# Optimization experiments

Measured on AMD Instinct MI355X. Metric: run time of the kernel, lower is better.

Reference implementation:

```python
import jax, jax.numpy as jnp
import numpy as np

NUM_EMBEDDINGS = 1024
EMBEDDING_DIM = 64
COMMITMENT_COST = 0.25

def setup_inputs() -> dict:
    key = jax.random.key(0)
    k1, k2 = jax.random.split(key)
    z = jax.random.normal(k1, (64, EMBEDDING_DIM, 32, 32), dtype=jnp.float32)
    # nn.Embedding initialized uniform(-1/K, 1/K)
    lim = 1.0 / NUM_EMBEDDINGS
    embeddings = jax.random.uniform(k2, (NUM_EMBEDDINGS, EMBEDDING_DIM), dtype=jnp.float32, minval=-lim, maxval=lim)
    return {"z": z, "embeddings": embeddings}

def reference(z, embeddings):
    # z: [B, C, H, W] with C == embedding_dim
    z_perm = jnp.transpose(z, (0, 2, 3, 1))            # [B, H, W, D]
    flat_z = z_perm.reshape(-1, EMBEDDING_DIM)          # [N, D]
    # squared L2 distances: ||z||^2 - 2 z.e + ||e||^2  -> [N, K]
    distances = (jnp.sum(flat_z ** 2, axis=1, keepdims=True)
                 - 2.0 * flat_z @ embeddings.T
                 + jnp.sum(embeddings ** 2, axis=1))
    encoding_indices = jnp.argmin(distances, axis=1)    # [N]
    # direct gather == one-hot @ embeddings (same math, no [N,K] one-hot)
    quantized = embeddings[encoding_indices].reshape(z_perm.shape)
    commitment_loss = COMMITMENT_COST * jnp.mean((jax.lax.stop_gradient(quantized) - z_perm) ** 2)
    codebook_loss = jnp.mean((quantized - jax.lax.stop_gradient(z_perm)) ** 2)
    loss = commitment_loss + codebook_loss
    # straight-through estimator
    quantized_st = z_perm + jax.lax.stop_gradient(quantized - z_perm)
    return jnp.transpose(quantized_st, (0, 3, 1, 2)), loss
```

## Files before the change

kernel.cpp:

```cpp
#include <hip/hip_runtime.h>

#define D 64
#define K 1024
#define NVEC 65536
#define MB 128
#define NBLK (NVEC / MB)
#define WAVES 4
#define KPW (K / WAVES)
#define TILES (KPW / 16)
#define NG (MB / 16)
#define RING 4

typedef __attribute__((ext_vector_type(8))) short bf16x8;
typedef __attribute__((ext_vector_type(4))) float f32x4;

__device__ inline unsigned pk2t(float a, float b) {
    return __builtin_amdgcn_perm(__builtin_bit_cast(unsigned, b),
                                 __builtin_bit_cast(unsigned, a), 0x07060302u);
}
__device__ inline int max3i(int a, int b, int c) {
    const int m = a > b ? a : b;
    return m > c ? m : c;
}

__global__ __launch_bounds__(256) void vq_prep(const float* __restrict__ emb,
                                               unsigned* __restrict__ ebf_u,
                                               float* __restrict__ hb) {
    const int r = blockIdx.x * 8 + (threadIdx.x >> 5);
    const int j = threadIdx.x & 31;
    const float2 v = *reinterpret_cast<const float2*>(emb + (size_t)r * D + j * 2);
    ebf_u[(size_t)r * 32 + j] = pk2t(v.x, v.y);
    float s = fmaf(v.x, v.x, v.y * v.y);
#pragma unroll
    for (int off = 1; off < 32; off <<= 1) s += __shfl_xor(s, off, 64);
    if (j == 0) hb[r] = 1.0f - 0.5f * s;
}

__global__ __launch_bounds__(256, 2) void vq_main(const float* __restrict__ z,
                                                  const float* __restrict__ emb,
                                                  const unsigned short* __restrict__ ebf,
                                                  const float* __restrict__ hb,
                                                  float* __restrict__ out,
                                                  float* __restrict__ pP) {
    __shared__ __align__(16) char zl[MB * 128];
    __shared__ int   wv[WAVES * MB];
    __shared__ int   fin[MB];
    __shared__ float redw[WAVES];

    const int tid = threadIdx.x;
    const int blk = blockIdx.x;
    const int b   = blk >> 3;
    const int hw0 = (blk & 7) * MB;
    const float* zb = z + (size_t)b * (D * 1024) + hw0;

    const int wave = tid >> 6;
    const int lane = tid & 63;
    const int cw   = wave * KPW;
    const int l16  = lane & 15;
    const int lg   = lane >> 4;

    float zacc = 0.f;
#pragma unroll
    for (int it = 0; it < 2; ++it) {
        const int item = it * 256 + tid;
        const int v4 = item & 31;
        const int d4 = item >> 5;
        float4 r[4];
#pragma unroll
        for (int i = 0; i < 4; ++i)
            r[i] = *reinterpret_cast<const float4*>(zb + (size_t)(d4 * 4 + i) * 1024 + v4 * 4);
        const float* rf = reinterpret_cast<const float*>(r);
#pragma unroll
        for (int n = 0; n < 16; ++n) zacc = fmaf(rf[n], rf[n], zacc);
#pragma unroll
        for (int j = 0; j < 4; ++j) {
            const int v = v4 * 4 + j;
            uint2 pk;
            pk.x = pk2t(rf[0 * 4 + j], rf[1 * 4 + j]);
            pk.y = pk2t(rf[2 * 4 + j], rf[3 * 4 + j]);
            const int byte = v * 128 + ((d4 * 8) ^ ((v & 7) << 4));
            *reinterpret_cast<uint2*>(zl + byte) = pk;
        }
    }

    bf16x8 A0[RING], A1[RING];
    f32x4  CI[RING];
#pragma unroll
    for (int p = 0; p < RING; ++p) {
        const unsigned short* row = ebf + (size_t)(cw + p * 16 + l16) * 64;
        A0[p] = *reinterpret_cast<const bf16x8*>(row + lg * 8);
        A1[p] = *reinterpret_cast<const bf16x8*>(row + 32 + lg * 8);
        CI[p] = *reinterpret_cast<const f32x4*>(hb + cw + p * 16 + lg * 4);
    }
    __syncthreads();

    bf16x8 bfr[NG][2];
#pragma unroll
    for (int g = 0; g < NG; ++g)
#pragma unroll
        for (int h = 0; h < 2; ++h) {
            const int v = g * 16 + l16;
            const int byte = v * 128 + (((h * 64) + lg * 16) ^ ((v & 7) << 4));
            bfr[g][h] = *reinterpret_cast<const bf16x8*>(zl + byte);
        }

    int best[NG];
#pragma unroll
    for (int g = 0; g < NG; ++g) best[g] = 0;

#pragma unroll 4
    for (int kt = 0; kt < TILES; ++kt) {
        const int cur = kt & (RING - 1);
        const bf16x8 b0 = A0[cur], b1 = A1[cur];
        const f32x4  cc = CI[cur];
        const int nk = (kt + RING < TILES) ? kt + RING : kt;
        const unsigned short* nrow = ebf + (size_t)(cw + nk * 16 + l16) * 64;
        A0[cur] = *reinterpret_cast<const bf16x8*>(nrow + lg * 8);
        A1[cur] = *reinterpret_cast<const bf16x8*>(nrow + 32 + lg * 8);
        CI[cur] = *reinterpret_cast<const f32x4*>(hb + cw + nk * 16 + lg * 4);

        const int idx0 = cw + kt * 16 + lg * 4;
#pragma unroll
        for (int g = 0; g < NG; ++g) {
            f32x4 c = cc;
            c = __builtin_amdgcn_mfma_f32_16x16x32_bf16(b0, bfr[g][0], c, 0, 0, 0);
            c = __builtin_amdgcn_mfma_f32_16x16x32_bf16(b1, bfr[g][1], c, 0, 0, 0);
            const int p0 = (int)((__builtin_bit_cast(unsigned, c[0]) & 0xFFFFFC00u) | (unsigned)(idx0 + 0));
            const int p1 = (int)((__builtin_bit_cast(unsigned, c[1]) & 0xFFFFFC00u) | (unsigned)(idx0 + 1));
            const int p2 = (int)((__builtin_bit_cast(unsigned, c[2]) & 0xFFFFFC00u) | (unsigned)(idx0 + 2));
            const int p3 = (int)((__builtin_bit_cast(unsigned, c[3]) & 0xFFFFFC00u) | (unsigned)(idx0 + 3));
            best[g] = max3i(max3i(p0, p1, p2), p3, best[g]);
        }
    }

#pragma unroll
    for (int g = 0; g < NG; ++g) {
        int tv = best[g];
        int o = __shfl_xor(tv, 16, 64); tv = tv > o ? tv : o;
        o = __shfl_xor(tv, 32, 64);     tv = tv > o ? tv : o;
        if (lane < 16) wv[wave * MB + g * 16 + l16] = tv;
    }
    __syncthreads();

    float tcon = 0.f;
    if (tid < MB) {
        int tv = wv[tid];
#pragma unroll
        for (int w = 1; w < WAVES; ++w) {
            const int o = wv[w * MB + tid];
            tv = tv > o ? tv : o;
        }
        fin[tid] = tv & (K - 1);
        tcon = __builtin_bit_cast(float, (unsigned)tv & 0xFFFFFC00u) - 1.0f;
    }
    __syncthreads();

    {
        const int v  = tid & 127;
        const int dh = tid >> 7;
        const int idx = fin[v];
        const float4* eq4 = reinterpret_cast<const float4*>(emb + (size_t)idx * D + dh * 32);
        float* ob = out + (size_t)b * (D * 1024) + hw0 + v;
#pragma unroll
        for (int i = 0; i < 8; ++i) {
            const float4 q = eq4[i];
            const int d = dh * 32 + i * 4;
            ob[(size_t)(d + 0) * 1024] = q.x;
            ob[(size_t)(d + 1) * 1024] = q.y;
            ob[(size_t)(d + 2) * 1024] = q.z;
            ob[(size_t)(d + 3) * 1024] = q.w;
        }
    }

    float s = zacc - 2.f * tcon;
#pragma unroll
    for (int off = 1; off < 64; off <<= 1) s += __shfl_xor(s, off, 64);
    if (lane == 0) redw[wave] = s;
    __syncthreads();
    if (tid == 0) pP[blk] = (redw[0] + redw[1]) + (redw[2] + redw[3]);
}

__global__ __launch_bounds__(256) void vq_loss(const float* __restrict__ pP,
                                               float* __restrict__ loss_out) {
    __shared__ float red[256];
    float s = 0.f;
    for (int i = threadIdx.x; i < NBLK; i += 256) s += pP[i];
    red[threadIdx.x] = s;
    __syncthreads();
#pragma unroll
    for (int st = 128; st > 0; st >>= 1) {
        if (threadIdx.x < st) red[threadIdx.x] += red[threadIdx.x + st];
        __syncthreads();
    }
    if (threadIdx.x == 0)
        loss_out[0] = 1.25f * red[0] * (1.0f / (float)((size_t)NVEC * D));
}

extern "C" void kernel_launch(void* const* d_in, const int* in_sizes, int n_in,
                              void* d_out, int out_size, void* d_ws, size_t ws_size,
                              hipStream_t stream) {
    const float* z   = (const float*)d_in[0];
    const float* emb = (const float*)d_in[1];
    float* out = (float*)d_out;

    char* ws = (char*)d_ws;
    unsigned* ebf_u = (unsigned*)ws;
    float* hb = (float*)(ws + 131072);
    float* pP = (float*)(ws + 135168);

    vq_prep<<<128, 256, 0, stream>>>(emb, ebf_u, hb);
    vq_main<<<NBLK, 256, 0, stream>>>(z, emb, (const unsigned short*)ebf_u, hb, out, pP);
    vq_loss<<<1, 256, 0, stream>>>(pP, out + (size_t)NVEC * D);
}
```

Baseline: 29.05 us.

## Fuse codebook bf16 conversion and norm computation into main kernel, drop prep launch

Removes the separate prep kernel that converted the codebook to bf16 and computed per-code half-norms. The main kernel now loads fp32 codebook rows directly, packs them to bf16 in registers and computes the norms with shuffles inside the k-tile loop. This saves one kernel launch and its workspace round trip, but every one of the 512 blocks now redoes the conversion and norm work and reads twice as many codebook bytes. The prefetch ring is reduced from 4 to 2 to offset the larger fp32 register footprint.

```diff
diff --git a/kernel.cpp b/kernel.cpp
--- a/kernel.cpp
+++ b/kernel.cpp
@@ -9,10 +9,11 @@
 #define KPW (K / WAVES)
 #define TILES (KPW / 16)
 #define NG (MB / 16)
-#define RING 4
+#define RING 2
 
 typedef __attribute__((ext_vector_type(8))) short bf16x8;
 typedef __attribute__((ext_vector_type(4))) float f32x4;
+typedef __attribute__((ext_vector_type(4))) int i32x4;
 
 __device__ inline unsigned pk2t(float a, float b) {
     return __builtin_amdgcn_perm(__builtin_bit_cast(unsigned, b),
@@ -22,24 +23,14 @@
     const int m = a > b ? a : b;
     return m > c ? m : c;
 }
-
-__global__ __launch_bounds__(256) void vq_prep(const float* __restrict__ emb,
-                                               unsigned* __restrict__ ebf_u,
-                                               float* __restrict__ hb) {
-    const int r = blockIdx.x * 8 + (threadIdx.x >> 5);
-    const int j = threadIdx.x & 31;
-    const float2 v = *reinterpret_cast<const float2*>(emb + (size_t)r * D + j * 2);
-    ebf_u[(size_t)r * 32 + j] = pk2t(v.x, v.y);
-    float s = fmaf(v.x, v.x, v.y * v.y);
-#pragma unroll
-    for (int off = 1; off < 32; off <<= 1) s += __shfl_xor(s, off, 64);
-    if (j == 0) hb[r] = 1.0f - 0.5f * s;
+__device__ inline float dot4(float4 v, float acc) {
+    acc = fmaf(v.x, v.x, acc); acc = fmaf(v.y, v.y, acc);
+    acc = fmaf(v.z, v.z, acc); acc = fmaf(v.w, v.w, acc);
+    return acc;
 }
 
 __global__ __launch_bounds__(256, 2) void vq_main(const float* __restrict__ z,
                                                   const float* __restrict__ emb,
-                                                  const unsigned short* __restrict__ ebf,
-                                                  const float* __restrict__ hb,
                                                   float* __restrict__ out,
                                                   float* __restrict__ pP) {
     __shared__ __align__(16) char zl[MB * 128];
@@ -83,14 +74,12 @@
         }
     }
 
-    bf16x8 A0[RING], A1[RING];
-    f32x4  CI[RING];
+    float4 F0[RING], F1[RING], F2[RING], F3[RING];
 #pragma unroll
     for (int p = 0; p < RING; ++p) {
-        const unsigned short* row = ebf + (size_t)(cw + p * 16 + l16) * 64;
-        A0[p] = *reinterpret_cast<const bf16x8*>(row + lg * 8);
-        A1[p] = *reinterpret_cast<const bf16x8*>(row + 32 + lg * 8);
-        CI[p] = *reinterpret_cast<const f32x4*>(hb + cw + p * 16 + lg * 4);
+        const float4* rp = reinterpret_cast<const float4*>(emb + (size_t)(cw + p * 16 + l16) * D);
+        F0[p] = rp[lg * 2];     F1[p] = rp[lg * 2 + 1];
+        F2[p] = rp[8 + lg * 2]; F3[p] = rp[8 + lg * 2 + 1];
     }
     __syncthreads();
 
@@ -108,23 +97,36 @@
 #pragma unroll
     for (int g = 0; g < NG; ++g) best[g] = 0;
 
-#pragma unroll 4
+#pragma unroll 2
     for (int kt = 0; kt < TILES; ++kt) {
         const int cur = kt & (RING - 1);
-        const bf16x8 b0 = A0[cur], b1 = A1[cur];
-        const f32x4  cc = CI[cur];
+        const float4 f0 = F0[cur], f1 = F1[cur], f2 = F2[cur], f3 = F3[cur];
         const int nk = (kt + RING < TILES) ? kt + RING : kt;
-        const unsigned short* nrow = ebf + (size_t)(cw + nk * 16 + l16) * 64;
-        A0[cur] = *reinterpret_cast<const bf16x8*>(nrow + lg * 8);
-        A1[cur] = *reinterpret_cast<const bf16x8*>(nrow + 32 + lg * 8);
-        CI[cur] = *reinterpret_cast<const f32x4*>(hb + cw + nk * 16 + lg * 4);
+        const float4* np = reinterpret_cast<const float4*>(emb + (size_t)(cw + nk * 16 + l16) * D);
+        F0[cur] = np[lg * 2];     F1[cur] = np[lg * 2 + 1];
+        F2[cur] = np[8 + lg * 2]; F3[cur] = np[8 + lg * 2 + 1];
+
+        i32x4 ai0 = { (int)pk2t(f0.x, f0.y), (int)pk2t(f0.z, f0.w),
+                      (int)pk2t(f1.x, f1.y), (int)pk2t(f1.z, f1.w) };
+        i32x4 ai1 = { (int)pk2t(f2.x, f2.y), (int)pk2t(f2.z, f2.w),
+                      (int)pk2t(f3.x, f3.y), (int)pk2t(f3.z, f3.w) };
+        const bf16x8 a0 = __builtin_bit_cast(bf16x8, ai0);
+        const bf16x8 a1 = __builtin_bit_cast(bf16x8, ai1);
+
+        float nrm = dot4(f3, dot4(f2, dot4(f1, dot4(f0, 0.f))));
+        nrm += __shfl_xor(nrm, 16, 64);
+        nrm += __shfl_xor(nrm, 32, 64);
+        f32x4 cc;
+#pragma unroll
+        for (int r = 0; r < 4; ++r)
+            cc[r] = fmaf(-0.5f, __shfl(nrm, lg * 4 + r, 16), 1.0f);
 
         const int idx0 = cw + kt * 16 + lg * 4;
 #pragma unroll
         for (int g = 0; g < NG; ++g) {
             f32x4 c = cc;
-            c = __builtin_amdgcn_mfma_f32_16x16x32_bf16(b0, bfr[g][0], c, 0, 0, 0);
-            c = __builtin_amdgcn_mfma_f32_16x16x32_bf16(b1, bfr[g][1], c, 0, 0, 0);
+            c = __builtin_amdgcn_mfma_f32_16x16x32_bf16(a0, bfr[g][0], c, 0, 0, 0);
+            c = __builtin_amdgcn_mfma_f32_16x16x32_bf16(a1, bfr[g][1], c, 0, 0, 0);
             const int p0 = (int)((__builtin_bit_cast(unsigned, c[0]) & 0xFFFFFC00u) | (unsigned)(idx0 + 0));
             const int p1 = (int)((__builtin_bit_cast(unsigned, c[1]) & 0xFFFFFC00u) | (unsigned)(idx0 + 1));
             const int p2 = (int)((__builtin_bit_cast(unsigned, c[2]) & 0xFFFFFC00u) | (unsigned)(idx0 + 2));
@@ -203,12 +205,8 @@
     const float* emb = (const float*)d_in[1];
     float* out = (float*)d_out;
 
-    char* ws = (char*)d_ws;
-    unsigned* ebf_u = (unsigned*)ws;
-    float* hb = (float*)(ws + 131072);
-    float* pP = (float*)(ws + 135168);
-
-    vq_prep<<<128, 256, 0, stream>>>(emb, ebf_u, hb);
-    vq_main<<<NBLK, 256, 0, stream>>>(z, emb, (const unsigned short*)ebf_u, hb, out, pP);
+    float* pP = (float*)d_ws;
+
+    vq_main<<<NBLK, 256, 0, stream>>>(z, emb, out, pP);
     vq_loss<<<1, 256, 0, stream>>>(pP, out + (size_t)NVEC * D);
 }
```

After: 29.63 us. About the same (+2.0%).

## Fuse loss reduction into main kernel via last-block atomic counter

Applied to the files above, without the earlier changes.

Drops the separate single-block loss kernel. Each block now publishes its partial sum atomically and bumps a global counter, and the last block to arrive does the final reduction. This removes one kernel launch and its serialization gap. The register prefetch ring is also cut from 4 to 2 with a smaller unroll, which lowers register pressure but shortens latency hiding for codebook loads. The counter is never reset and relies on a modulo of the block count, so it assumes the workspace starts at zero and NBLK is a power of two.

```diff
diff --git a/kernel.cpp b/kernel.cpp
--- a/kernel.cpp
+++ b/kernel.cpp
@@ -9,7 +9,7 @@
 #define KPW (K / WAVES)
 #define TILES (KPW / 16)
 #define NG (MB / 16)
-#define RING 4
+#define RING 2
 
 typedef __attribute__((ext_vector_type(8))) short bf16x8;
 typedef __attribute__((ext_vector_type(4))) float f32x4;
@@ -41,11 +41,14 @@
                                                   const unsigned short* __restrict__ ebf,
                                                   const float* __restrict__ hb,
                                                   float* __restrict__ out,
-                                                  float* __restrict__ pP) {
+                                                  unsigned* __restrict__ pPu,
+                                                  unsigned* __restrict__ counter) {
     __shared__ __align__(16) char zl[MB * 128];
     __shared__ int   wv[WAVES * MB];
     __shared__ int   fin[MB];
     __shared__ float redw[WAVES];
+    __shared__ float red2[256];
+    __shared__ int   amLastS;
 
     const int tid = threadIdx.x;
     const int blk = blockIdx.x;
@@ -108,7 +111,7 @@
 #pragma unroll
     for (int g = 0; g < NG; ++g) best[g] = 0;
 
-#pragma unroll 4
+#pragma unroll 2
     for (int kt = 0; kt < TILES; ++kt) {
         const int cur = kt & (RING - 1);
         const bf16x8 b0 = A0[cur], b1 = A1[cur];
@@ -177,23 +180,33 @@
     for (int off = 1; off < 64; off <<= 1) s += __shfl_xor(s, off, 64);
     if (lane == 0) redw[wave] = s;
     __syncthreads();
-    if (tid == 0) pP[blk] = (redw[0] + redw[1]) + (redw[2] + redw[3]);
-}
-
-__global__ __launch_bounds__(256) void vq_loss(const float* __restrict__ pP,
-                                               float* __restrict__ loss_out) {
-    __shared__ float red[256];
-    float s = 0.f;
-    for (int i = threadIdx.x; i < NBLK; i += 256) s += pP[i];
-    red[threadIdx.x] = s;
-    __syncthreads();
-#pragma unroll
-    for (int st = 128; st > 0; st >>= 1) {
-        if (threadIdx.x < st) red[threadIdx.x] += red[threadIdx.x + st];
+
+    if (tid == 0) {
+        const float part = (redw[0] + redw[1]) + (redw[2] + redw[3]);
+        atomicExch(&pPu[blk], __builtin_bit_cast(unsigned, part));
+        __threadfence();
+        const unsigned old = atomicAdd(counter, 1u);
+        amLastS = ((old & (NBLK - 1)) == (NBLK - 1));
+    }
+    __syncthreads();
+
+    if (amLastS) {
+        float sum = 0.f;
+#pragma unroll
+        for (int rep = 0; rep < NBLK / 256; ++rep) {
+            const unsigned ub = atomicAdd(&pPu[rep * 256 + tid], 0u);
+            sum += __builtin_bit_cast(float, ub);
+        }
+        red2[tid] = sum;
         __syncthreads();
-    }
-    if (threadIdx.x == 0)
-        loss_out[0] = 1.25f * red[0] * (1.0f / (float)((size_t)NVEC * D));
+#pragma unroll
+        for (int st = 128; st > 0; st >>= 1) {
+            if (tid < st) red2[tid] += red2[tid + st];
+            __syncthreads();
+        }
+        if (tid == 0)
+            out[(size_t)NVEC * D] = 1.25f * red2[0] * (1.0f / (float)((size_t)NVEC * D));
+    }
 }
 
 extern "C" void kernel_launch(void* const* d_in, const int* in_sizes, int n_in,
@@ -204,11 +217,12 @@
     float* out = (float*)d_out;
 
     char* ws = (char*)d_ws;
-    unsigned* ebf_u = (unsigned*)ws;
-    float* hb = (float*)(ws + 131072);
-    float* pP = (float*)(ws + 135168);
+    unsigned* ebf_u   = (unsigned*)ws;
+    float* hb         = (float*)(ws + 131072);
+    unsigned* pPu     = (unsigned*)(ws + 135168);
+    unsigned* counter = (unsigned*)(ws + 137216);
 
     vq_prep<<<128, 256, 0, stream>>>(emb, ebf_u, hb);
-    vq_main<<<NBLK, 256, 0, stream>>>(z, emb, (const unsigned short*)ebf_u, hb, out, pP);
-    vq_loss<<<1, 256, 0, stream>>>(pP, out + (size_t)NVEC * D);
-}
+    vq_main<<<NBLK, 256, 0, stream>>>(z, emb, (const unsigned short*)ebf_u, hb,
+                                      out, pPu, counter);
+}
```

New measurement: 41.79 us. 1.44x slower.

## Switch distance GEMM from 16x16x32 to 32x32x16 bf16 MFMA tiles

Applied to the files above, without the earlier changes.

Replaces the 16x16x32 MFMA tiling of the codebook-by-vector distance product with 32x32x16 MFMA tiles. Each wave now handles 32 codes by 32 vectors per tile, which changes the register fragment layout, the prefetch ring (depth 2 with four A fragments per stage) and the cross-lane reduction. The intent is a higher ratio of MFMA work to VALU argmin packing and loads, since each accumulator register now carries more useful work per instruction. It raises register pressure (16-wide accumulators, larger ring and fragments), which could hurt occupancy at the 2-blocks launch bound.

```diff
diff --git a/kernel.cpp b/kernel.cpp
--- a/kernel.cpp
+++ b/kernel.cpp
@@ -7,12 +7,13 @@
 #define NBLK (NVEC / MB)
 #define WAVES 4
 #define KPW (K / WAVES)
-#define TILES (KPW / 16)
-#define NG (MB / 16)
-#define RING 4
+#define TILES (KPW / 32)
+#define NG (MB / 32)
+#define RING 2
 
 typedef __attribute__((ext_vector_type(8))) short bf16x8;
 typedef __attribute__((ext_vector_type(4))) float f32x4;
+typedef __attribute__((ext_vector_type(16))) float f32x16;
 
 __device__ inline unsigned pk2t(float a, float b) {
     return __builtin_amdgcn_perm(__builtin_bit_cast(unsigned, b),
@@ -56,8 +57,8 @@
     const int wave = tid >> 6;
     const int lane = tid & 63;
     const int cw   = wave * KPW;
-    const int l16  = lane & 15;
-    const int lg   = lane >> 4;
+    const int l32  = lane & 31;
+    const int hi   = lane >> 5;
 
     float zacc = 0.f;
 #pragma unroll
@@ -83,62 +84,87 @@
         }
     }
 
-    bf16x8 A0[RING], A1[RING];
-    f32x4  CI[RING];
+    bf16x8 A[RING][4];
+    f32x4  CI[RING][4];
 #pragma unroll
     for (int p = 0; p < RING; ++p) {
-        const unsigned short* row = ebf + (size_t)(cw + p * 16 + l16) * 64;
-        A0[p] = *reinterpret_cast<const bf16x8*>(row + lg * 8);
-        A1[p] = *reinterpret_cast<const bf16x8*>(row + 32 + lg * 8);
-        CI[p] = *reinterpret_cast<const f32x4*>(hb + cw + p * 16 + lg * 4);
-    }
-    __syncthreads();
-
-    bf16x8 bfr[NG][2];
+        const unsigned short* row = ebf + (size_t)(cw + p * 32 + l32) * 64 + hi * 8;
+#pragma unroll
+        for (int s = 0; s < 4; ++s)
+            A[p][s] = *reinterpret_cast<const bf16x8*>(row + s * 16);
+        const float* hrow = hb + cw + p * 32 + 4 * hi;
+#pragma unroll
+        for (int q = 0; q < 4; ++q)
+            CI[p][q] = *reinterpret_cast<const f32x4*>(hrow + q * 8);
+    }
+    __syncthreads();
+
+    bf16x8 bfr[NG][4];
 #pragma unroll
     for (int g = 0; g < NG; ++g)
 #pragma unroll
-        for (int h = 0; h < 2; ++h) {
-            const int v = g * 16 + l16;
-            const int byte = v * 128 + (((h * 64) + lg * 16) ^ ((v & 7) << 4));
-            bfr[g][h] = *reinterpret_cast<const bf16x8*>(zl + byte);
+        for (int s = 0; s < 4; ++s) {
+            const int v = g * 32 + l32;
+            const int byte = v * 128 + (((s * 32) + hi * 16) ^ ((v & 7) << 4));
+            bfr[g][s] = *reinterpret_cast<const bf16x8*>(zl + byte);
         }
 
     int best[NG];
 #pragma unroll
     for (int g = 0; g < NG; ++g) best[g] = 0;
 
-#pragma unroll 4
+#pragma unroll
     for (int kt = 0; kt < TILES; ++kt) {
         const int cur = kt & (RING - 1);
-        const bf16x8 b0 = A0[cur], b1 = A1[cur];
-        const f32x4  cc = CI[cur];
+        bf16x8 a0 = A[cur][0], a1 = A[cur][1], a2 = A[cur][2], a3 = A[cur][3];
+        f32x16 cc;
+#pragma unroll
+        for (int q = 0; q < 4; ++q) {
+            cc[q * 4 + 0] = CI[cur][q][0];
+            cc[q * 4 + 1] = CI[cur][q][1];
+            cc[q * 4 + 2] = CI[cur][q][2];
+            cc[q * 4 + 3] = CI[cur][q][3];
+        }
         const int nk = (kt + RING < TILES) ? kt + RING : kt;
-        const unsigned short* nrow = ebf + (size_t)(cw + nk * 16 + l16) * 64;
-        A0[cur] = *reinterpret_cast<const bf16x8*>(nrow + lg * 8);
-        A1[cur] = *reinterpret_cast<const bf16x8*>(nrow + 32 + lg * 8);
-        CI[cur] = *reinterpret_cast<const f32x4*>(hb + cw + nk * 16 + lg * 4);
-
-        const int idx0 = cw + kt * 16 + lg * 4;
+        {
+            const unsigned short* nrow = ebf + (size_t)(cw + nk * 32 + l32) * 64 + hi * 8;
+#pragma unroll
+            for (int s = 0; s < 4; ++s)
+                A[cur][s] = *reinterpret_cast<const bf16x8*>(nrow + s * 16);
+            const float* hrow = hb + cw + nk * 32 + 4 * hi;
+#pragma unroll
+            for (int q = 0; q < 4; ++q)
+                CI[cur][q] = *reinterpret_cast<const f32x4*>(hrow + q * 8);
+        }
+
+        const int idx0 = cw + kt * 32 + 4 * hi;
 #pragma unroll
         for (int g = 0; g < NG; ++g) {
-            f32x4 c = cc;
-            c = __builtin_amdgcn_mfma_f32_16x16x32_bf16(b0, bfr[g][0], c, 0, 0, 0);
-            c = __builtin_amdgcn_mfma_f32_16x16x32_bf16(b1, bfr[g][1], c, 0, 0, 0);
-            const int p0 = (int)((__builtin_bit_cast(unsigned, c[0]) & 0xFFFFFC00u) | (unsigned)(idx0 + 0));
-            const int p1 = (int)((__builtin_bit_cast(unsigned, c[1]) & 0xFFFFFC00u) | (unsigned)(idx0 + 1));
-            const int p2 = (int)((__builtin_bit_cast(unsigned, c[2]) & 0xFFFFFC00u) | (unsigned)(idx0 + 2));
-            const int p3 = (int)((__builtin_bit_cast(unsigned, c[3]) & 0xFFFFFC00u) | (unsigned)(idx0 + 3));
-            best[g] = max3i(max3i(p0, p1, p2), p3, best[g]);
+            f32x16 c = cc;
+            c = __builtin_amdgcn_mfma_f32_32x32x16_bf16(a0, bfr[g][0], c, 0, 0, 0);
+            c = __builtin_amdgcn_mfma_f32_32x32x16_bf16(a1, bfr[g][1], c, 0, 0, 0);
+            c = __builtin_amdgcn_mfma_f32_32x32x16_bf16(a2, bfr[g][2], c, 0, 0, 0);
+            c = __builtin_amdgcn_mfma_f32_32x32x16_bf16(a3, bfr[g][3], c, 0, 0, 0);
+            int p[16];
+#pragma unroll
+            for (int r = 0; r < 16; ++r)
+                p[r] = (int)((__builtin_bit_cast(unsigned, c[r]) & 0xFFFFFC00u)
+                             | (unsigned)(idx0 + (r & 3) + 8 * (r >> 2)));
+            const int m0 = max3i(p[0],  p[1],  p[2]);
+            const int m1 = max3i(p[3],  p[4],  p[5]);
+            const int m2 = max3i(p[6],  p[7],  p[8]);
+            const int m3 = max3i(p[9],  p[10], p[11]);
+            const int m4 = max3i(p[12], p[13], p[14]);
+            best[g] = max3i(max3i(m0, m1, m2), max3i(m3, m4, p[15]), best[g]);
         }
     }
 
 #pragma unroll
     for (int g = 0; g < NG; ++g) {
         int tv = best[g];
-        int o = __shfl_xor(tv, 16, 64); tv = tv > o ? tv : o;
-        o = __shfl_xor(tv, 32, 64);     tv = tv > o ? tv : o;
-        if (lane < 16) wv[wave * MB + g * 16 + l16] = tv;
+        const int o = __shfl_xor(tv, 32, 64);
+        tv = tv > o ? tv : o;
+        if (lane < 32) wv[wave * MB + g * 32 + l32] = tv;
     }
     __syncthreads();
 
```

After: 36.91 us. +27.0%, slower.
